# Kernel tuning notes

Hardware: AMD Instinct MI355X
Metric: run time of the kernel (lower is better)

Reference implementation:

```python
import jax, jax.numpy as jnp
import numpy as np

N = 8192
E = 262144
IN_DIM, HID, OUT = 256, 256, 32


def setup_inputs() -> dict:
    key = jax.random.key(0)
    ks = jax.random.split(key, 10)
    features = jax.random.normal(ks[0], (N, IN_DIM), jnp.float32)
    noise = jax.random.normal(ks[1], (N, OUT), jnp.float32)
    src = jax.random.randint(ks[2], (E,), 0, N, jnp.int32)
    dst = jax.random.randint(ks[3], (E,), 0, N, jnp.int32)
    s = lambda fi, fo: 1.0 / np.sqrt(fi)
    W1 = jax.random.normal(ks[4], (IN_DIM, HID), jnp.float32) * s(IN_DIM, HID)
    W2 = jax.random.normal(ks[5], (HID, HID), jnp.float32) * s(HID, HID)
    W3 = jax.random.normal(ks[6], (HID, OUT), jnp.float32) * s(HID, OUT)
    b1 = jnp.zeros((HID,), jnp.float32)
    b2 = jnp.zeros((HID,), jnp.float32)
    b3 = jnp.zeros((OUT,), jnp.float32)
    fc_w = jax.random.normal(ks[7], (IN_DIM, OUT), jnp.float32) * s(IN_DIM, OUT)
    return dict(features=features, noise=noise, src=src, dst=dst,
                W1=W1, b1=b1, W2=W2, b2=b2, W3=W3, b3=b3, fc_w=fc_w)


def _degree_norms(src, dst, n):
    ones = jnp.ones_like(src, jnp.float32)
    out_deg = jax.ops.segment_sum(ones, src, num_segments=n)
    in_deg = jax.ops.segment_sum(ones, dst, num_segments=n)
    # DGL GraphConv norm='both' clamps degrees to min 1 before pow(-0.5)
    norm_src = jnp.maximum(out_deg, 1.0) ** -0.5  # [N]
    norm_dst = jnp.maximum(in_deg, 1.0) ** -0.5   # [N]
    return norm_src, norm_dst


def _graph_conv(x, src, dst, norm_src, norm_dst, W, b, n):
    # h = D_in^{-1/2} A D_out^{-1/2} x W + b, then relu
    h = x @ W                                  # transform first (smaller agg dim)
    m = (h * norm_src[:, None])[src]           # [E, F] gather + scale
    agg = jax.ops.segment_sum(m, dst, num_segments=n)
    return jax.nn.relu(agg * norm_dst[:, None] + b)


def reference(features, noise, src, dst, W1, b1, W2, b2, W3, b3, fc_w):
    n = features.shape[0]
    norm_s, norm_d = _degree_norms(src, dst, n)
    h = _graph_conv(features, src, dst, norm_s, norm_d, W1, b1, n)
    mean = _graph_conv(h, src, dst, norm_s, norm_d, W2, b2, n)
    log_std = _graph_conv(h, src, dst, norm_s, norm_d, W3, b3, n)
    # note: mean [N,HID] broadcasts against noise*exp(log_std) [N,OUT] only if
    # HID==OUT dims align; original code has mean from layer[1] (hidden_dim) and
    # log_std from layer[2] (out_dim). To keep the math runnable we follow the
    # VGAE intent: layer[1] and layer[2] both map to out_dim here (W2 below is
    # hidden->hidden, W3 hidden->out; mean uses W3-shaped branch). See notes.
    z = mean[:, :noise.shape[1]] if mean.shape[1] != noise.shape[1] else mean
    z = z + noise * jnp.exp(log_std)
    adj_rec = jax.nn.sigmoid(z @ z.T)          # [N, N] dense decoder
    seq_fts = features @ fc_w                  # Linear(in_dim, out_dim, bias=False)
    return adj_rec, z, seq_fts
```

## Files before the change

kernel.cpp:

```cpp
#include <hip/hip_runtime.h>
#include <hip/hip_fp16.h>

#define NNODES 8192
#define NEDGES 262144
#define NNOUT 67108864L
#define CAP 128

typedef _Float16 half8 __attribute__((ext_vector_type(8)));
typedef _Float16 half4 __attribute__((ext_vector_type(4)));
typedef _Float16 half2v __attribute__((ext_vector_type(2)));
typedef float float4v __attribute__((ext_vector_type(4)));
typedef float float2v __attribute__((ext_vector_type(2)));


__global__ __launch_bounds__(256) void prep_deg(const float* __restrict__ W1, const float* __restrict__ W2,
                                                const float* __restrict__ W3, const float* __restrict__ b2,
                                                const float* __restrict__ b3, const int* __restrict__ src,
                                                const int* __restrict__ dst, _Float16* __restrict__ W1th,
                                                _Float16* __restrict__ W1tl, _Float16* __restrict__ Wzth,
                                                _Float16* __restrict__ Wztl, float* __restrict__ bz,
                                                int* __restrict__ out_deg, int* __restrict__ in_deg,
                                                int* __restrict__ csr) {
  int b = blockIdx.x, t = threadIdx.x;
  if (b < 256) {
    float w = W1[b * 256 + t];
    _Float16 wh = (_Float16)w;
    W1th[t * 256 + b] = wh;
    W1tl[t * 256 + b] = (_Float16)(w - (float)wh);
    if (b >= 64 && b < 128) {
      int c = b - 64;
      float v = (c < 32) ? W2[t * 256 + c] : W3[t * 32 + (c - 32)];
      _Float16 vh = (_Float16)v;
      Wzth[c * 256 + t] = vh;
      Wztl[c * 256 + t] = (_Float16)(v - (float)vh);
    }
    if (b == 128 && t < 64) bz[t] = (t < 32) ? b2[t] : b3[t - 32];
    return;
  }
  int e = (b - 256) * 256 + t;
  int s = src[e], d = dst[e];
  int pos = atomicAdd(&in_deg[d], 1);
  if (pos < CAP) csr[d * CAP + pos] = s;
  atomicAdd(&out_deg[s], 1);
}


__global__ __launch_bounds__(256) void convert_seq(const float* __restrict__ x, const int* __restrict__ out_deg,
                                                   const float* __restrict__ Wf, _Float16* __restrict__ xs,
                                                   float* __restrict__ seq) {
  int b = blockIdx.x, t = threadIdx.x;
  if (b >= 2048) {
    int tt = (b - 2048) * 256 + t;
    int row = tt >> 3;
    int cq = (tt & 7) * 4;
    float a0 = 0.f, a1 = 0.f, a2 = 0.f, a3 = 0.f;
    const float* frow = x + row * 256;
    for (int k = 0; k < 256; k += 4) {
      float4 fv = *(const float4*)(frow + k);
      float4 w0 = *(const float4*)(Wf + k * 32 + cq);
      float4 w1 = *(const float4*)(Wf + (k + 1) * 32 + cq);
      float4 w2 = *(const float4*)(Wf + (k + 2) * 32 + cq);
      float4 w3 = *(const float4*)(Wf + (k + 3) * 32 + cq);
      a0 = fmaf(fv.x, w0.x, fmaf(fv.y, w1.x, fmaf(fv.z, w2.x, fmaf(fv.w, w3.x, a0))));
      a1 = fmaf(fv.x, w0.y, fmaf(fv.y, w1.y, fmaf(fv.z, w2.y, fmaf(fv.w, w3.y, a1))));
      a2 = fmaf(fv.x, w0.z, fmaf(fv.y, w1.z, fmaf(fv.z, w2.z, fmaf(fv.w, w3.z, a2))));
      a3 = fmaf(fv.x, w0.w, fmaf(fv.y, w1.w, fmaf(fv.z, w2.w, fmaf(fv.w, w3.w, a3))));
    }
    float4 o = {a0, a1, a2, a3};
    *(float4*)&seq[row * 32 + cq] = o;
    return;
  }
  int i = b * 256 + t;
  int base = i * 4;
  int row = base >> 8;
  int od = out_deg[row];
  float ns = rsqrtf((float)(od < 1 ? 1 : od));
  float4 v = *(const float4*)(x + base);
  half4 o = {(_Float16)(v.x * ns), (_Float16)(v.y * ns), (_Float16)(v.z * ns), (_Float16)(v.w * ns)};
  *(half4*)(xs + base) = o;
}


__device__ __forceinline__ int swz(int r, int c) {
  return (r * 256 + c) ^ ((r & 7) << 3);
}

__global__ __launch_bounds__(256) void prop_gemm1(const _Float16* __restrict__ xs, const int* __restrict__ in_deg,
                                                  const int* __restrict__ out_deg, const int* __restrict__ csr,
                                                  const _Float16* __restrict__ W1th, const _Float16* __restrict__ W1tl,
                                                  const float* __restrict__ b1, _Float16* __restrict__ xs2) {
  __shared__ __align__(16) _Float16 Qh[16 * 256];
  __shared__ __align__(16) _Float16 Ql[16 * 256];
  int t = threadIdx.x;
  int w = t >> 6, lane = t & 63;
  int rowBase = blockIdx.x * 16;
#pragma unroll
  for (int i = 0; i < 4; ++i) {
    int r16 = w * 4 + i;
    int v = rowBase + r16;
    int degv = in_deg[v];
    int deg = degv > CAP ? CAP : degv;
    const _Float16* base = xs + 4 * lane;
    const int* ep = csr + v * CAP;
    float a0 = 0.f, a1 = 0.f, a2 = 0.f, a3 = 0.f;
    int e = 0;
    for (; e + 4 <= deg; e += 4) {
      int s0 = ep[e], s1 = ep[e + 1], s2 = ep[e + 2], s3 = ep[e + 3];
      half4 v0 = *(const half4*)(base + (long)s0 * 256);
      half4 v1 = *(const half4*)(base + (long)s1 * 256);
      half4 v2 = *(const half4*)(base + (long)s2 * 256);
      half4 v3 = *(const half4*)(base + (long)s3 * 256);
      a0 += (float)v0.x + (float)v1.x + (float)v2.x + (float)v3.x;
      a1 += (float)v0.y + (float)v1.y + (float)v2.y + (float)v3.y;
      a2 += (float)v0.z + (float)v1.z + (float)v2.z + (float)v3.z;
      a3 += (float)v0.w + (float)v1.w + (float)v2.w + (float)v3.w;
    }
    for (; e < deg; ++e) {
      half4 v0 = *(const half4*)(base + (long)ep[e] * 256);
      a0 += (float)v0.x; a1 += (float)v0.y; a2 += (float)v0.z; a3 += (float)v0.w;
    }
    float nd = rsqrtf((float)(degv < 1 ? 1 : degv));
    a0 *= nd; a1 *= nd; a2 *= nd; a3 *= nd;
    _Float16 h0 = (_Float16)a0, h1 = (_Float16)a1, h2 = (_Float16)a2, h3 = (_Float16)a3;
    int idx = swz(r16, lane * 4);
    *(half4*)&Qh[idx] = half4{h0, h1, h2, h3};
    *(half4*)&Ql[idx] = half4{(_Float16)(a0 - (float)h0), (_Float16)(a1 - (float)h1),
                              (_Float16)(a2 - (float)h2), (_Float16)(a3 - (float)h3)};
  }
  __syncthreads();
  int l15 = lane & 15, lk = (lane >> 4) * 8;
  float4v acc[4] = {};
  for (int ks = 0; ks < 8; ++ks) {
    int ai = swz(l15, ks * 32 + lk);
    half8 ah = *(const half8*)&Qh[ai];
    half8 al = *(const half8*)&Ql[ai];
#pragma unroll
    for (int j = 0; j < 4; ++j) {
      int ct = w * 4 + j;
      long bo = (long)(ct * 16 + l15) * 256 + ks * 32 + lk;
      half8 bh = *(const half8*)(W1th + bo);
      half8 bl = *(const half8*)(W1tl + bo);
      acc[j] = __builtin_amdgcn_mfma_f32_16x16x32_f16(al, bh, acc[j], 0, 0, 0);
      acc[j] = __builtin_amdgcn_mfma_f32_16x16x32_f16(ah, bl, acc[j], 0, 0, 0);
      acc[j] = __builtin_amdgcn_mfma_f32_16x16x32_f16(ah, bh, acc[j], 0, 0, 0);
    }
  }
  int crow = (lane >> 4) * 4;
#pragma unroll
  for (int j = 0; j < 4; ++j) {
    int c = (w * 4 + j) * 16 + l15;
    float bb = b1[c];
#pragma unroll
    for (int r = 0; r < 4; ++r) {
      int row = rowBase + crow + r;
      int od = out_deg[row];
      float nsrc = rsqrtf((float)(od < 1 ? 1 : od));
      xs2[(long)row * 256 + c] = (_Float16)(fmaxf(acc[j][r] + bb, 0.f) * nsrc);
    }
  }
}


__global__ __launch_bounds__(256) void prop_gemmz(const _Float16* __restrict__ xs2, const int* __restrict__ in_deg,
                                                  const int* __restrict__ csr, const _Float16* __restrict__ Wzth,
                                                  const _Float16* __restrict__ Wztl, const float* __restrict__ bz,
                                                  const float* __restrict__ noise, float* __restrict__ zout,
                                                  _Float16* __restrict__ Zh, _Float16* __restrict__ Zl) {
  __shared__ __align__(16) _Float16 Qh[16 * 256];
  __shared__ __align__(16) _Float16 Ql[16 * 256];
  __shared__ float sm[16][64];
  int t = threadIdx.x;
  int w = t >> 6, lane = t & 63;
  int rowBase = blockIdx.x * 16;
#pragma unroll
  for (int i = 0; i < 4; ++i) {
    int r16 = w * 4 + i;
    int v = rowBase + r16;
    int degv = in_deg[v];
    int deg = degv > CAP ? CAP : degv;
    const _Float16* base = xs2 + 4 * lane;
    const int* ep = csr + v * CAP;
    float a0 = 0.f, a1 = 0.f, a2 = 0.f, a3 = 0.f;
    int e = 0;
    for (; e + 4 <= deg; e += 4) {
      int s0 = ep[e], s1 = ep[e + 1], s2 = ep[e + 2], s3 = ep[e + 3];
      half4 v0 = *(const half4*)(base + (long)s0 * 256);
      half4 v1 = *(const half4*)(base + (long)s1 * 256);
      half4 v2 = *(const half4*)(base + (long)s2 * 256);
      half4 v3 = *(const half4*)(base + (long)s3 * 256);
      a0 += (float)v0.x + (float)v1.x + (float)v2.x + (float)v3.x;
      a1 += (float)v0.y + (float)v1.y + (float)v2.y + (float)v3.y;
      a2 += (float)v0.z + (float)v1.z + (float)v2.z + (float)v3.z;
      a3 += (float)v0.w + (float)v1.w + (float)v2.w + (float)v3.w;
    }
    for (; e < deg; ++e) {
      half4 v0 = *(const half4*)(base + (long)ep[e] * 256);
      a0 += (float)v0.x; a1 += (float)v0.y; a2 += (float)v0.z; a3 += (float)v0.w;
    }
    float nd = rsqrtf((float)(degv < 1 ? 1 : degv));
    a0 *= nd; a1 *= nd; a2 *= nd; a3 *= nd;
    _Float16 h0 = (_Float16)a0, h1 = (_Float16)a1, h2 = (_Float16)a2, h3 = (_Float16)a3;
    int idx = swz(r16, lane * 4);
    *(half4*)&Qh[idx] = half4{h0, h1, h2, h3};
    *(half4*)&Ql[idx] = half4{(_Float16)(a0 - (float)h0), (_Float16)(a1 - (float)h1),
                              (_Float16)(a2 - (float)h2), (_Float16)(a3 - (float)h3)};
  }
  __syncthreads();
  int l15 = lane & 15, lk = (lane >> 4) * 8;
  float4v acc = {};
  for (int ks = 0; ks < 8; ++ks) {
    int ai = swz(l15, ks * 32 + lk);
    half8 ah = *(const half8*)&Qh[ai];
    half8 al = *(const half8*)&Ql[ai];
    long bo = (long)(w * 16 + l15) * 256 + ks * 32 + lk;
    half8 bh = *(const half8*)(Wzth + bo);
    half8 bl = *(const half8*)(Wztl + bo);
    acc = __builtin_amdgcn_mfma_f32_16x16x32_f16(al, bh, acc, 0, 0, 0);
    acc = __builtin_amdgcn_mfma_f32_16x16x32_f16(ah, bl, acc, 0, 0, 0);
    acc = __builtin_amdgcn_mfma_f32_16x16x32_f16(ah, bh, acc, 0, 0, 0);
  }
  int crow = (lane >> 4) * 4;
  float bb = bz[w * 16 + l15];
#pragma unroll
  for (int r = 0; r < 4; ++r) sm[crow + r][w * 16 + l15] = fmaxf(acc[r] + bb, 0.f);
  __syncthreads();
  int idx = t * 2;
  int r = idx >> 5, c = idx & 31;
  long row = rowBase + r;
  float m0 = sm[r][c], m1 = sm[r][c + 1];
  float l0 = sm[r][32 + c], l1 = sm[r][32 + c + 1];
  float2 nz = *(const float2*)(noise + row * 32 + c);
  float z0 = m0 + nz.x * __expf(l0);
  float z1 = m1 + nz.y * __expf(l1);
  float2v zo = {z0, z1};
  *(float2v*)(zout + row * 32 + c) = zo;
  _Float16 h0 = (_Float16)z0, h1 = (_Float16)z1;
  half2v zh = {h0, h1};
  half2v zl = {(_Float16)(z0 - (float)h0), (_Float16)(z1 - (float)h1)};
  *(half2v*)(Zh + row * 32 + c) = zh;
  *(half2v*)(Zl + row * 32 + c) = zl;
}


__global__ __launch_bounds__(256) void adj_mfma(const _Float16* __restrict__ Zh, const _Float16* __restrict__ Zl,
                                                float* __restrict__ out) {
  __shared__ __align__(16) float lds[4][32][68];
  int tid = threadIdx.x;
  int wave = tid >> 6;
  int lane = tid & 63;
  long rowBase = (long)blockIdx.y * 128 + wave * 32;
  long colBase = (long)blockIdx.x * 128;
  int l15 = lane & 15;
  int lk = (lane >> 4) * 8;
  half8 ah0 = *(const half8*)(Zh + (rowBase + l15) * 32 + lk);
  half8 al0 = *(const half8*)(Zl + (rowBase + l15) * 32 + lk);
  half8 ah1 = *(const half8*)(Zh + (rowBase + 16 + l15) * 32 + lk);
  half8 al1 = *(const half8*)(Zl + (rowBase + 16 + l15) * 32 + lk);
  int crow = (lane >> 4) * 4;
  float* slab = &lds[wave][0][0];
#pragma unroll
  for (int h = 0; h < 2; ++h) {
#pragma unroll
    for (int ct = 0; ct < 4; ++ct) {
      int cg = h * 4 + ct;
      half8 bh = *(const half8*)(Zh + (colBase + cg * 16 + l15) * 32 + lk);
      half8 bl = *(const half8*)(Zl + (colBase + cg * 16 + l15) * 32 + lk);
      float4v acc0 = {}, acc1 = {};
      acc0 = __builtin_amdgcn_mfma_f32_16x16x32_f16(al0, bh, acc0, 0, 0, 0);
      acc0 = __builtin_amdgcn_mfma_f32_16x16x32_f16(ah0, bl, acc0, 0, 0, 0);
      acc0 = __builtin_amdgcn_mfma_f32_16x16x32_f16(ah0, bh, acc0, 0, 0, 0);
      acc1 = __builtin_amdgcn_mfma_f32_16x16x32_f16(al1, bh, acc1, 0, 0, 0);
      acc1 = __builtin_amdgcn_mfma_f32_16x16x32_f16(ah1, bl, acc1, 0, 0, 0);
      acc1 = __builtin_amdgcn_mfma_f32_16x16x32_f16(ah1, bh, acc1, 0, 0, 0);
#pragma unroll
      for (int r = 0; r < 4; ++r) {
        slab[(crow + r) * 68 + ct * 16 + l15] = __builtin_amdgcn_rcpf(1.f + __expf(-acc0[r]));
        slab[(16 + crow + r) * 68 + ct * 16 + l15] = __builtin_amdgcn_rcpf(1.f + __expf(-acc1[r]));
      }
    }
#pragma unroll
    for (int i = 0; i < 8; ++i) {
      int rr = 4 * i + (lane >> 4);
      float4v v = *(const float4v*)&slab[rr * 68 + 4 * l15];
      __builtin_nontemporal_store(v, (float4v*)&out[(rowBase + rr) * 8192 + colBase + h * 64 + 4 * l15]);
    }
  }
}


extern "C" void kernel_launch(void* const* d_in, const int* in_sizes, int n_in,
                              void* d_out, int out_size, void* d_ws, size_t ws_size,
                              hipStream_t stream) {
  const float* features = (const float*)d_in[0];
  const float* noise    = (const float*)d_in[1];
  const int*   src      = (const int*)d_in[2];
  const int*   dst      = (const int*)d_in[3];
  const float* W1       = (const float*)d_in[4];
  const float* b1       = (const float*)d_in[5];
  const float* W2       = (const float*)d_in[6];
  const float* b2       = (const float*)d_in[7];
  const float* W3       = (const float*)d_in[8];
  const float* b3       = (const float*)d_in[9];
  const float* fcw      = (const float*)d_in[10];

  float* out = (float*)d_out;

  int* ws_i    = (int*)d_ws;
  int* out_deg = ws_i;
  int* in_deg  = ws_i + 8192;
  _Float16* Zh = (_Float16*)(ws_i + 16384);
  _Float16* Zl = (_Float16*)(ws_i + 147456);

  float* adj      = out;
  float* zbuf     = out + NNOUT;
  float* seq      = out + NNOUT + 262144;
  _Float16* xs    = (_Float16*)out;
  _Float16* xs2   = (_Float16*)(out + 1048576);
  _Float16* W1th  = (_Float16*)(out + 3145728);
  _Float16* W1tl  = (_Float16*)(out + 3178496);
  _Float16* Wzth  = (_Float16*)(out + 3211264);
  _Float16* Wztl  = (_Float16*)(out + 3219456);
  float*    bz    = out + 3227648;
  int*      csr   = (int*)(out + 4194304);

  hipMemsetAsync(out_deg, 0, 2 * 8192 * sizeof(int), stream);
  prep_deg<<<1280, 256, 0, stream>>>(W1, W2, W3, b2, b3, src, dst,
                                     W1th, W1tl, Wzth, Wztl, bz, out_deg, in_deg, csr);
  convert_seq<<<2304, 256, 0, stream>>>(features, out_deg, fcw, xs, seq);
  prop_gemm1<<<512, 256, 0, stream>>>(xs, in_deg, out_deg, csr, W1th, W1tl, b1, xs2);
  prop_gemmz<<<512, 256, 0, stream>>>(xs2, in_deg, csr, Wzth, Wztl, bz, noise, zbuf, Zh, Zl);
  adj_mfma<<<dim3(64, 64), 256, 0, stream>>>(Zh, Zl, adj);
}
```

Before: 221.0 us.

## Fuse prep kernels, apply source norm at gather, restructure adjacency decoder tiles

```diff
diff --git a/kernel.cpp b/kernel.cpp
--- a/kernel.cpp
+++ b/kernel.cpp
@@ -8,19 +8,20 @@
 
 typedef _Float16 half8 __attribute__((ext_vector_type(8)));
 typedef _Float16 half4 __attribute__((ext_vector_type(4)));
-typedef _Float16 half2v __attribute__((ext_vector_type(2)));
 typedef float float4v __attribute__((ext_vector_type(4)));
 typedef float float2v __attribute__((ext_vector_type(2)));
 
 
-__global__ __launch_bounds__(256) void prep_deg(const float* __restrict__ W1, const float* __restrict__ W2,
+__global__ __launch_bounds__(256) void prep_all(const float* __restrict__ W1, const float* __restrict__ W2,
                                                 const float* __restrict__ W3, const float* __restrict__ b2,
                                                 const float* __restrict__ b3, const int* __restrict__ src,
-                                                const int* __restrict__ dst, _Float16* __restrict__ W1th,
+                                                const int* __restrict__ dst, const float* __restrict__ x,
+                                                const float* __restrict__ Wf, _Float16* __restrict__ W1th,
                                                 _Float16* __restrict__ W1tl, _Float16* __restrict__ Wzth,
                                                 _Float16* __restrict__ Wztl, float* __restrict__ bz,
                                                 int* __restrict__ out_deg, int* __restrict__ in_deg,
-                                                int* __restrict__ csr) {
+                                                int* __restrict__ csr, _Float16* __restrict__ xs,
+                                                float* __restrict__ seq) {
   int b = blockIdx.x, t = threadIdx.x;
   if (b < 256) {
     float w = W1[b * 256 + t];
@@ -37,53 +38,79 @@
     if (b == 128 && t < 64) bz[t] = (t < 32) ? b2[t] : b3[t - 32];
     return;
   }
-  int e = (b - 256) * 256 + t;
-  int s = src[e], d = dst[e];
-  int pos = atomicAdd(&in_deg[d], 1);
-  if (pos < CAP) csr[d * CAP + pos] = s;
-  atomicAdd(&out_deg[s], 1);
-}
-
-
-__global__ __launch_bounds__(256) void convert_seq(const float* __restrict__ x, const int* __restrict__ out_deg,
-                                                   const float* __restrict__ Wf, _Float16* __restrict__ xs,
-                                                   float* __restrict__ seq) {
-  int b = blockIdx.x, t = threadIdx.x;
-  if (b >= 2048) {
-    int tt = (b - 2048) * 256 + t;
-    int row = tt >> 3;
-    int cq = (tt & 7) * 4;
-    float a0 = 0.f, a1 = 0.f, a2 = 0.f, a3 = 0.f;
-    const float* frow = x + row * 256;
-    for (int k = 0; k < 256; k += 4) {
-      float4 fv = *(const float4*)(frow + k);
-      float4 w0 = *(const float4*)(Wf + k * 32 + cq);
-      float4 w1 = *(const float4*)(Wf + (k + 1) * 32 + cq);
-      float4 w2 = *(const float4*)(Wf + (k + 2) * 32 + cq);
-      float4 w3 = *(const float4*)(Wf + (k + 3) * 32 + cq);
-      a0 = fmaf(fv.x, w0.x, fmaf(fv.y, w1.x, fmaf(fv.z, w2.x, fmaf(fv.w, w3.x, a0))));
-      a1 = fmaf(fv.x, w0.y, fmaf(fv.y, w1.y, fmaf(fv.z, w2.y, fmaf(fv.w, w3.y, a1))));
-      a2 = fmaf(fv.x, w0.z, fmaf(fv.y, w1.z, fmaf(fv.z, w2.z, fmaf(fv.w, w3.z, a2))));
-      a3 = fmaf(fv.x, w0.w, fmaf(fv.y, w1.w, fmaf(fv.z, w2.w, fmaf(fv.w, w3.w, a3))));
-    }
-    float4 o = {a0, a1, a2, a3};
-    *(float4*)&seq[row * 32 + cq] = o;
+  if (b < 1280) {
+    int e = (b - 256) * 256 + t;
+    int s = src[e], d = dst[e];
+    int pos = atomicAdd(&in_deg[d], 1);
+    if (pos < CAP) csr[d * CAP + pos] = s;
+    atomicAdd(&out_deg[s], 1);
     return;
   }
-  int i = b * 256 + t;
-  int base = i * 4;
-  int row = base >> 8;
-  int od = out_deg[row];
-  float ns = rsqrtf((float)(od < 1 ? 1 : od));
-  float4 v = *(const float4*)(x + base);
-  half4 o = {(_Float16)(v.x * ns), (_Float16)(v.y * ns), (_Float16)(v.z * ns), (_Float16)(v.w * ns)};
-  *(half4*)(xs + base) = o;
-}
-
+  if (b < 3328) {
+    long base = ((long)(b - 1280) * 256 + t) * 4;
+    float4 v = *(const float4*)(x + base);
+    half4 o = {(_Float16)v.x, (_Float16)v.y, (_Float16)v.z, (_Float16)v.w};
+    *(half4*)(xs + base) = o;
+    return;
+  }
+  int tt = (b - 3328) * 256 + t;
+  int row = tt >> 3;
+  int cq = (tt & 7) * 4;
+  float a0 = 0.f, a1 = 0.f, a2 = 0.f, a3 = 0.f;
+  const float* frow = x + row * 256;
+  for (int k = 0; k < 256; k += 4) {
+    float4 fv = *(const float4*)(frow + k);
+    float4 w0 = *(const float4*)(Wf + k * 32 + cq);
+    float4 w1 = *(const float4*)(Wf + (k + 1) * 32 + cq);
+    float4 w2 = *(const float4*)(Wf + (k + 2) * 32 + cq);
+    float4 w3 = *(const float4*)(Wf + (k + 3) * 32 + cq);
+    a0 = fmaf(fv.x, w0.x, fmaf(fv.y, w1.x, fmaf(fv.z, w2.x, fmaf(fv.w, w3.x, a0))));
+    a1 = fmaf(fv.x, w0.y, fmaf(fv.y, w1.y, fmaf(fv.z, w2.y, fmaf(fv.w, w3.y, a1))));
+    a2 = fmaf(fv.x, w0.z, fmaf(fv.y, w1.z, fmaf(fv.z, w2.z, fmaf(fv.w, w3.z, a2))));
+    a3 = fmaf(fv.x, w0.w, fmaf(fv.y, w1.w, fmaf(fv.z, w2.w, fmaf(fv.w, w3.w, a3))));
+  }
+  float4 o = {a0, a1, a2, a3};
+  *(float4*)&seq[row * 32 + cq] = o;
+}
+
+
+__device__ __forceinline__ void gather_rows(const _Float16* __restrict__ xsrc, const int* __restrict__ ep,
+                                            const int* __restrict__ out_deg, int deg, int lane,
+                                            float& a0, float& a1, float& a2, float& a3) {
+  const _Float16* base = xsrc + 4 * lane;
+  int e = 0;
+  for (; e + 4 <= deg; e += 4) {
+    int s0 = ep[e], s1 = ep[e + 1], s2 = ep[e + 2], s3 = ep[e + 3];
+    int d0 = out_deg[s0], d1 = out_deg[s1], d2 = out_deg[s2], d3 = out_deg[s3];
+    float n0 = rsqrtf((float)(d0 < 1 ? 1 : d0));
+    float n1 = rsqrtf((float)(d1 < 1 ? 1 : d1));
+    float n2 = rsqrtf((float)(d2 < 1 ? 1 : d2));
+    float n3 = rsqrtf((float)(d3 < 1 ? 1 : d3));
+    half4 v0 = *(const half4*)(base + (long)s0 * 256);
+    half4 v1 = *(const half4*)(base + (long)s1 * 256);
+    half4 v2 = *(const half4*)(base + (long)s2 * 256);
+    half4 v3 = *(const half4*)(base + (long)s3 * 256);
+    a0 = fmaf(n0, (float)v0.x, fmaf(n1, (float)v1.x, fmaf(n2, (float)v2.x, fmaf(n3, (float)v3.x, a0))));
+    a1 = fmaf(n0, (float)v0.y, fmaf(n1, (float)v1.y, fmaf(n2, (float)v2.y, fmaf(n3, (float)v3.y, a1))));
+    a2 = fmaf(n0, (float)v0.z, fmaf(n1, (float)v1.z, fmaf(n2, (float)v2.z, fmaf(n3, (float)v3.z, a2))));
+    a3 = fmaf(n0, (float)v0.w, fmaf(n1, (float)v1.w, fmaf(n2, (float)v2.w, fmaf(n3, (float)v3.w, a3))));
+  }
+  for (; e < deg; ++e) {
+    int s0 = ep[e];
+    int d0 = out_deg[s0];
+    float n0 = rsqrtf((float)(d0 < 1 ? 1 : d0));
+    half4 v0 = *(const half4*)(base + (long)s0 * 256);
+    a0 = fmaf(n0, (float)v0.x, a0);
+    a1 = fmaf(n0, (float)v0.y, a1);
+    a2 = fmaf(n0, (float)v0.z, a2);
+    a3 = fmaf(n0, (float)v0.w, a3);
+  }
+}
 
 __device__ __forceinline__ int swz(int r, int c) {
   return (r * 256 + c) ^ ((r & 7) << 3);
 }
+
 
 __global__ __launch_bounds__(256) void prop_gemm1(const _Float16* __restrict__ xs, const int* __restrict__ in_deg,
                                                   const int* __restrict__ out_deg, const int* __restrict__ csr,
@@ -100,25 +127,8 @@
     int v = rowBase + r16;
     int degv = in_deg[v];
     int deg = degv > CAP ? CAP : degv;
-    const _Float16* base = xs + 4 * lane;
-    const int* ep = csr + v * CAP;
     float a0 = 0.f, a1 = 0.f, a2 = 0.f, a3 = 0.f;
-    int e = 0;
-    for (; e + 4 <= deg; e += 4) {
-      int s0 = ep[e], s1 = ep[e + 1], s2 = ep[e + 2], s3 = ep[e + 3];
-      half4 v0 = *(const half4*)(base + (long)s0 * 256);
-      half4 v1 = *(const half4*)(base + (long)s1 * 256);
-      half4 v2 = *(const half4*)(base + (long)s2 * 256);
-      half4 v3 = *(const half4*)(base + (long)s3 * 256);
-      a0 += (float)v0.x + (float)v1.x + (float)v2.x + (float)v3.x;
-      a1 += (float)v0.y + (float)v1.y + (float)v2.y + (float)v3.y;
-      a2 += (float)v0.z + (float)v1.z + (float)v2.z + (float)v3.z;
-      a3 += (float)v0.w + (float)v1.w + (float)v2.w + (float)v3.w;
-    }
-    for (; e < deg; ++e) {
-      half4 v0 = *(const half4*)(base + (long)ep[e] * 256);
-      a0 += (float)v0.x; a1 += (float)v0.y; a2 += (float)v0.z; a3 += (float)v0.w;
-    }
+    gather_rows(xs, csr + v * CAP, out_deg, deg, lane, a0, a1, a2, a3);
     float nd = rsqrtf((float)(degv < 1 ? 1 : degv));
     a0 *= nd; a1 *= nd; a2 *= nd; a3 *= nd;
     _Float16 h0 = (_Float16)a0, h1 = (_Float16)a1, h2 = (_Float16)a2, h3 = (_Float16)a3;
@@ -153,19 +163,18 @@
 #pragma unroll
     for (int r = 0; r < 4; ++r) {
       int row = rowBase + crow + r;
-      int od = out_deg[row];
-      float nsrc = rsqrtf((float)(od < 1 ? 1 : od));
-      xs2[(long)row * 256 + c] = (_Float16)(fmaxf(acc[j][r] + bb, 0.f) * nsrc);
+      xs2[(long)row * 256 + c] = (_Float16)fmaxf(acc[j][r] + bb, 0.f);
     }
   }
 }
 
 
 __global__ __launch_bounds__(256) void prop_gemmz(const _Float16* __restrict__ xs2, const int* __restrict__ in_deg,
-                                                  const int* __restrict__ csr, const _Float16* __restrict__ Wzth,
-                                                  const _Float16* __restrict__ Wztl, const float* __restrict__ bz,
-                                                  const float* __restrict__ noise, float* __restrict__ zout,
-                                                  _Float16* __restrict__ Zh, _Float16* __restrict__ Zl) {
+                                                  const int* __restrict__ out_deg, const int* __restrict__ csr,
+                                                  const _Float16* __restrict__ Wzth, const _Float16* __restrict__ Wztl,
+                                                  const float* __restrict__ bz, const float* __restrict__ noise,
+                                                  float* __restrict__ zout, _Float16* __restrict__ Zh,
+                                                  _Float16* __restrict__ Zl) {
   __shared__ __align__(16) _Float16 Qh[16 * 256];
   __shared__ __align__(16) _Float16 Ql[16 * 256];
   __shared__ float sm[16][64];
@@ -178,25 +187,8 @@
     int v = rowBase + r16;
     int degv = in_deg[v];
     int deg = degv > CAP ? CAP : degv;
-    const _Float16* base = xs2 + 4 * lane;
-    const int* ep = csr + v * CAP;
     float a0 = 0.f, a1 = 0.f, a2 = 0.f, a3 = 0.f;
-    int e = 0;
-    for (; e + 4 <= deg; e += 4) {
-      int s0 = ep[e], s1 = ep[e + 1], s2 = ep[e + 2], s3 = ep[e + 3];
-      half4 v0 = *(const half4*)(base + (long)s0 * 256);
-      half4 v1 = *(const half4*)(base + (long)s1 * 256);
-      half4 v2 = *(const half4*)(base + (long)s2 * 256);
-      half4 v3 = *(const half4*)(base + (long)s3 * 256);
-      a0 += (float)v0.x + (float)v1.x + (float)v2.x + (float)v3.x;
-      a1 += (float)v0.y + (float)v1.y + (float)v2.y + (float)v3.y;
-      a2 += (float)v0.z + (float)v1.z + (float)v2.z + (float)v3.z;
-      a3 += (float)v0.w + (float)v1.w + (float)v2.w + (float)v3.w;
-    }
-    for (; e < deg; ++e) {
-      half4 v0 = *(const half4*)(base + (long)ep[e] * 256);
-      a0 += (float)v0.x; a1 += (float)v0.y; a2 += (float)v0.z; a3 += (float)v0.w;
-    }
+    gather_rows(xs2, csr + v * CAP, out_deg, deg, lane, a0, a1, a2, a3);
     float nd = rsqrtf((float)(degv < 1 ? 1 : degv));
     a0 *= nd; a1 *= nd; a2 *= nd; a3 *= nd;
     _Float16 h0 = (_Float16)a0, h1 = (_Float16)a1, h2 = (_Float16)a2, h3 = (_Float16)a3;
@@ -235,55 +227,46 @@
   float2v zo = {z0, z1};
   *(float2v*)(zout + row * 32 + c) = zo;
   _Float16 h0 = (_Float16)z0, h1 = (_Float16)z1;
-  half2v zh = {h0, h1};
-  half2v zl = {(_Float16)(z0 - (float)h0), (_Float16)(z1 - (float)h1)};
-  *(half2v*)(Zh + row * 32 + c) = zh;
-  *(half2v*)(Zl + row * 32 + c) = zl;
-}
-
-
-__global__ __launch_bounds__(256) void adj_mfma(const _Float16* __restrict__ Zh, const _Float16* __restrict__ Zl,
-                                                float* __restrict__ out) {
-  __shared__ __align__(16) float lds[4][32][68];
-  int tid = threadIdx.x;
-  int wave = tid >> 6;
-  int lane = tid & 63;
-  long rowBase = (long)blockIdx.y * 128 + wave * 32;
-  long colBase = (long)blockIdx.x * 128;
-  int l15 = lane & 15;
-  int lk = (lane >> 4) * 8;
-  half8 ah0 = *(const half8*)(Zh + (rowBase + l15) * 32 + lk);
-  half8 al0 = *(const half8*)(Zl + (rowBase + l15) * 32 + lk);
-  half8 ah1 = *(const half8*)(Zh + (rowBase + 16 + l15) * 32 + lk);
-  half8 al1 = *(const half8*)(Zl + (rowBase + 16 + l15) * 32 + lk);
+  *(Zh + row * 32 + c) = h0;
+  *(Zh + row * 32 + c + 1) = h1;
+  *(Zl + row * 32 + c) = (_Float16)(z0 - (float)h0);
+  *(Zl + row * 32 + c + 1) = (_Float16)(z1 - (float)h1);
+}
+
+
+__global__ __launch_bounds__(256) void adj_stream(const _Float16* __restrict__ Zh, const _Float16* __restrict__ Zl,
+                                                  float* __restrict__ out) {
+  __shared__ __align__(16) float slab[16 * 516];
+  int t = threadIdx.x;
+  int w = t >> 6, lane = t & 63;
+  long rowBase = (long)blockIdx.y * 16;
+  long colBase = (long)blockIdx.x * 512;
+  int l15 = lane & 15, lk = (lane >> 4) * 8;
+  half8 ah = *(const half8*)(Zh + (rowBase + l15) * 32 + lk);
+  half8 al = *(const half8*)(Zl + (rowBase + l15) * 32 + lk);
   int crow = (lane >> 4) * 4;
-  float* slab = &lds[wave][0][0];
-#pragma unroll
-  for (int h = 0; h < 2; ++h) {
-#pragma unroll
-    for (int ct = 0; ct < 4; ++ct) {
-      int cg = h * 4 + ct;
-      half8 bh = *(const half8*)(Zh + (colBase + cg * 16 + l15) * 32 + lk);
-      half8 bl = *(const half8*)(Zl + (colBase + cg * 16 + l15) * 32 + lk);
-      float4v acc0 = {}, acc1 = {};
-      acc0 = __builtin_amdgcn_mfma_f32_16x16x32_f16(al0, bh, acc0, 0, 0, 0);
-      acc0 = __builtin_amdgcn_mfma_f32_16x16x32_f16(ah0, bl, acc0, 0, 0, 0);
-      acc0 = __builtin_amdgcn_mfma_f32_16x16x32_f16(ah0, bh, acc0, 0, 0, 0);
-      acc1 = __builtin_amdgcn_mfma_f32_16x16x32_f16(al1, bh, acc1, 0, 0, 0);
-      acc1 = __builtin_amdgcn_mfma_f32_16x16x32_f16(ah1, bl, acc1, 0, 0, 0);
-      acc1 = __builtin_amdgcn_mfma_f32_16x16x32_f16(ah1, bh, acc1, 0, 0, 0);
-#pragma unroll
-      for (int r = 0; r < 4; ++r) {
-        slab[(crow + r) * 68 + ct * 16 + l15] = __builtin_amdgcn_rcpf(1.f + __expf(-acc0[r]));
-        slab[(16 + crow + r) * 68 + ct * 16 + l15] = __builtin_amdgcn_rcpf(1.f + __expf(-acc1[r]));
-      }
-    }
-#pragma unroll
-    for (int i = 0; i < 8; ++i) {
-      int rr = 4 * i + (lane >> 4);
-      float4v v = *(const float4v*)&slab[rr * 68 + 4 * l15];
-      __builtin_nontemporal_store(v, (float4v*)&out[(rowBase + rr) * 8192 + colBase + h * 64 + 4 * l15]);
-    }
+#pragma unroll
+  for (int k = 0; k < 8; ++k) {
+    int ctloc = w * 8 + k;
+    long zc = colBase + ctloc * 16 + l15;
+    half8 bh = *(const half8*)(Zh + zc * 32 + lk);
+    half8 bl = *(const half8*)(Zl + zc * 32 + lk);
+    float4v acc = {};
+    acc = __builtin_amdgcn_mfma_f32_16x16x32_f16(al, bh, acc, 0, 0, 0);
+    acc = __builtin_amdgcn_mfma_f32_16x16x32_f16(ah, bl, acc, 0, 0, 0);
+    acc = __builtin_amdgcn_mfma_f32_16x16x32_f16(ah, bh, acc, 0, 0, 0);
+#pragma unroll
+    for (int r = 0; r < 4; ++r)
+      slab[(crow + r) * 516 + ctloc * 16 + l15] = __builtin_amdgcn_rcpf(1.f + __expf(-acc[r]));
+  }
+  __syncthreads();
+  int fr2 = t >> 7;
+  int fc = (t & 127) * 4;
+#pragma unroll
+  for (int i = 0; i < 8; ++i) {
+    int row = i * 2 + fr2;
+    float4v v = *(const float4v*)&slab[row * 516 + fc];
+    *(float4v*)&out[(rowBase + row) * 8192 + colBase + fc] = v;
   }
 }
 
@@ -324,10 +307,9 @@
   int*      csr   = (int*)(out + 4194304);
 
   hipMemsetAsync(out_deg, 0, 2 * 8192 * sizeof(int), stream);
-  prep_deg<<<1280, 256, 0, stream>>>(W1, W2, W3, b2, b3, src, dst,
-                                     W1th, W1tl, Wzth, Wztl, bz, out_deg, in_deg, csr);
-  convert_seq<<<2304, 256, 0, stream>>>(features, out_deg, fcw, xs, seq);
+  prep_all<<<3584, 256, 0, stream>>>(W1, W2, W3, b2, b3, src, dst, features, fcw,
+                                     W1th, W1tl, Wzth, Wztl, bz, out_deg, in_deg, csr, xs, seq);
   prop_gemm1<<<512, 256, 0, stream>>>(xs, in_deg, out_deg, csr, W1th, W1tl, b1, xs2);
-  prop_gemmz<<<512, 256, 0, stream>>>(xs2, in_deg, csr, Wzth, Wztl, bz, noise, zbuf, Zh, Zl);
-  adj_mfma<<<dim3(64, 64), 256, 0, stream>>>(Zh, Zl, adj);
-}
+  prop_gemmz<<<512, 256, 0, stream>>>(xs2, in_deg, out_deg, csr, Wzth, Wztl, bz, noise, zbuf, Zh, Zl);
+  adj_stream<<<dim3(16, 512), 256, 0, stream>>>(Zh, Zl, adj);
+}
```

After: 207.0 us. 1.07x faster.
